# Optimization experiments

Hardware: AMD Instinct MI355X
Metric: run time of the kernel (lower is better)

Reference implementation:

```python
import jax, jax.numpy as jnp
import numpy as np

MAX_SHIFT_BANDS = 2.0


def setup_inputs() -> dict:
    key = jax.random.key(0)
    k1, k2 = jax.random.split(key)
    B, Bh, H, W = 4, 128, 256, 256
    x = jax.random.normal(k1, (B, Bh, H, W), dtype=jnp.float32)
    wavelength_shift = jax.random.normal(k2, (B, Bh, W), dtype=jnp.float32)
    return {"x": x, "wavelength_shift": wavelength_shift}


def reference(x, wavelength_shift):
    # Faithful to torch grid_sample(mode='bilinear', padding_mode='border',
    # align_corners=False) applied along the spectral (band) axis only.
    B, Bh, H, W = x.shape
    dt = x.dtype

    shift = jnp.clip(wavelength_shift, -MAX_SHIFT_BANDS, MAX_SHIFT_BANDS)
    shift = shift[:, :, None, :]                         # [B,Bh,1,W]
    band = jnp.arange(Bh, dtype=dt)[None, :, None, None]  # [1,Bh,1,1]
    shifted = jnp.clip(band + shift, 0.0, Bh - 1)        # [B,Bh,1,W]

    # grid_sample align_corners=False unnormalization:
    # grid g = shifted/(Bh-1)*2 - 1 ; iy = ((g+1)*Bh - 1)/2 = shifted*Bh/(Bh-1) - 0.5
    iy = shifted * (Bh / (Bh - 1)) - 0.5                 # [B,Bh,1,W]
    i0f = jnp.floor(iy)
    w = iy - i0f                                          # lerp weight, [B,Bh,1,W]
    i0 = i0f.astype(jnp.int32)                            # may be -1 at low edge
    i0c = jnp.clip(i0, 0, Bh - 1)                         # border padding
    i1c = jnp.clip(i0 + 1, 0, Bh - 1)

    # broadcast gather indices over H rows
    i0c = jnp.broadcast_to(i0c, (B, Bh, H, W))
    i1c = jnp.broadcast_to(i1c, (B, Bh, H, W))

    x0 = jnp.take_along_axis(x, i0c, axis=1)              # [B,Bh,H,W]
    x1 = jnp.take_along_axis(x, i1c, axis=1)
    return x0 * (1.0 - w) + x1 * w
```

## Files before the change

### kernel.cpp

```cpp
#include <hip/hip_runtime.h>


#define BH_ 128
#define H_  256
#define W_  256
#define TB   16
#define NLDS (TB + 6)

__global__ __launch_bounds__(256) void smile_kernel(
    const float* __restrict__ x,
    const float* __restrict__ ws,
    float* __restrict__ out)
{
    __shared__ float tile[NLDS][W_];

    const int t = threadIdx.x;
    int bid = blockIdx.x;
    const int tileI = bid & 7;
    bid >>= 3;
    const int h = bid & (H_ - 1);
    const int b = bid >> 8;
    const int bh0 = tileI * TB;

    const float* __restrict__ xsrc = x + (size_t)b * (BH_ * H_ * W_) + h * W_;
    for (int item = t; item < NLDS * (W_ / 4); item += 256) {
        const int i = item >> 6;
        const int q = item & 63;
        const int band = min(max(bh0 - 3 + i, 0), BH_ - 1);
        const float4 v = *reinterpret_cast<const float4*>(
            &xsrc[(size_t)band * (H_ * W_) + q * 4]);
        *reinterpret_cast<float4*>(&tile[i][q * 4]) = v;
    }
    __syncthreads();

    const float scale = (float)(128.0 / 127.0);
    const int w = t;
    const float* __restrict__ wsb = ws + (size_t)(b * BH_) * W_;
    float* __restrict__ outb =
        out + (((size_t)b * BH_ + bh0) * H_ + h) * W_;

#pragma unroll 4
    for (int r = 0; r < TB; ++r) {
        const int bh = bh0 + r;
        float s       = wsb[bh * W_ + w];
        float sc      = fminf(fmaxf(s, -2.0f), 2.0f);
        float shifted = fminf(fmaxf((float)bh + sc, 0.0f), (float)(BH_ - 1));
        float iy      = shifted * scale - 0.5f;
        float i0f     = floorf(iy);
        float frac    = iy - i0f;
        int   i0      = (int)i0f;
        int   i0c     = min(max(i0, 0), BH_ - 1);
        int   i1c     = min(i0 + 1, BH_ - 1);
        float x0 = tile[i0c - bh0 + 3][w];
        float x1 = tile[i1c - bh0 + 3][w];
        outb[(size_t)r * (H_ * W_) + w] = x0 * (1.0f - frac) + x1 * frac;
    }
}

extern "C" void kernel_launch(void* const* d_in, const int* in_sizes, int n_in,
                              void* d_out, int out_size, void* d_ws, size_t ws_size,
                              hipStream_t stream) {
    const float* x  = (const float*)d_in[0];
    const float* ws = (const float*)d_in[1];
    float* out = (float*)d_out;

    const int grid = 4 * H_ * (BH_ / TB);
    smile_kernel<<<grid, 256, 0, stream>>>(x, ws, out);
}
```

Before: 55.25 us.

## Load x tile straight into LDS and batch the shift loads ahead of compute

The register round-trip staging of x into shared memory is replaced with direct global-to-LDS loads (global_load_lds, 16 bytes per lane), with each wave filling whole band rows. All sixteen wavelength_shift values per thread are loaded up front into registers and the loop is fully unrolled, so the loads can overlap. The lerp is rewritten as a single fma. The aim is to cut VGPR traffic and instruction count in the staging phase and expose more memory-level parallelism, at the cost of depending on the gfx950 16-byte LDS DMA builtin and its lane-contiguous layout.

```diff
diff --git a/kernel.cpp b/kernel.cpp
--- a/kernel.cpp
+++ b/kernel.cpp
@@ -23,37 +23,43 @@
     const int bh0 = tileI * TB;
 
     const float* __restrict__ xsrc = x + (size_t)b * (BH_ * H_ * W_) + h * W_;
-    for (int item = t; item < NLDS * (W_ / 4); item += 256) {
-        const int i = item >> 6;
-        const int q = item & 63;
+    const int wave = t >> 6;
+    const int lane = t & 63;
+    for (int i = wave; i < NLDS; i += 4) {
         const int band = min(max(bh0 - 3 + i, 0), BH_ - 1);
-        const float4 v = *reinterpret_cast<const float4*>(
-            &xsrc[(size_t)band * (H_ * W_) + q * 4]);
-        *reinterpret_cast<float4*>(&tile[i][q * 4]) = v;
+        const float* gp = xsrc + (size_t)band * (H_ * W_) + lane * 4;
+        __builtin_amdgcn_global_load_lds(
+            (const __attribute__((address_space(1))) void*)gp,
+            (__attribute__((address_space(3))) void*)&tile[i][0],
+            16, 0, 0);
     }
     __syncthreads();
 
     const float scale = (float)(128.0 / 127.0);
     const int w = t;
-    const float* __restrict__ wsb = ws + (size_t)(b * BH_) * W_;
+    const float* __restrict__ wsb = ws + (size_t)(b * BH_ + bh0) * W_ + w;
     float* __restrict__ outb =
-        out + (((size_t)b * BH_ + bh0) * H_ + h) * W_;
+        out + (((size_t)b * BH_ + bh0) * H_ + h) * W_ + w;
 
-#pragma unroll 4
+    float s[TB];
+#pragma unroll
+    for (int r = 0; r < TB; ++r)
+        s[r] = wsb[r * W_];
+
+#pragma unroll
     for (int r = 0; r < TB; ++r) {
         const int bh = bh0 + r;
-        float s       = wsb[bh * W_ + w];
-        float sc      = fminf(fmaxf(s, -2.0f), 2.0f);
+        float sc      = fminf(fmaxf(s[r], -2.0f), 2.0f);
         float shifted = fminf(fmaxf((float)bh + sc, 0.0f), (float)(BH_ - 1));
-        float iy      = shifted * scale - 0.5f;
+        float iy      = fmaf(shifted, scale, -0.5f);
         float i0f     = floorf(iy);
         float frac    = iy - i0f;
         int   i0      = (int)i0f;
-        int   i0c     = min(max(i0, 0), BH_ - 1);
-        int   i1c     = min(i0 + 1, BH_ - 1);
-        float x0 = tile[i0c - bh0 + 3][w];
-        float x1 = tile[i1c - bh0 + 3][w];
-        outb[(size_t)r * (H_ * W_) + w] = x0 * (1.0f - frac) + x1 * frac;
+        int   r0      = min(max(i0, 0), BH_ - 1) - bh0 + 3;
+        int   r1      = min(i0 + 1, BH_ - 1) - bh0 + 3;
+        float x0 = tile[r0][w];
+        float x1 = tile[r1][w];
+        outb[(size_t)r * (H_ * W_)] = fmaf(frac, x1 - x0, x0);
     }
 }
 
```

Measured after the change: 50.65 us. 8.3% less time.
